# Performance work log

Measured on AMD Instinct MI355X. Metric: run time of the kernel, lower is better.

The kernel has to match this reference:

```python
import jax, jax.numpy as jnp
import numpy as np

WINDOW_SIZE = 11
SIGMA = 1.5
CHANNELS = 3
DATA_RANGE = 1.0


def _create_window(window_size, channel):
    x = np.arange(window_size) - window_size // 2
    g = np.exp(-(x ** 2) / (2.0 * SIGMA ** 2))
    g = g / g.sum()
    w2d = np.outer(g, g).astype(np.float32)  # [ws, ws]
    # depthwise kernel, OIHW with I=1, O=channel
    return jnp.asarray(np.broadcast_to(w2d, (channel, 1, window_size, window_size)).copy())


def _depthwise_conv(x, window, channel):
    # x: [B, C, H, W], window: [C, 1, ws, ws], VALID padding, groups=C
    return jax.lax.conv_general_dilated(
        x, window, window_strides=(1, 1), padding='VALID',
        dimension_numbers=('NCHW', 'OIHW', 'NCHW'),
        feature_group_count=channel)


def setup_inputs() -> dict:
    key = jax.random.key(0)
    k1, k2 = jax.random.split(key)
    img1 = jax.random.uniform(k1, (32, CHANNELS, 512, 512), dtype=jnp.float32)
    img2 = jax.random.uniform(k2, (32, CHANNELS, 512, 512), dtype=jnp.float32)
    return {"img1": img1, "img2": img2}


def reference(img1, img2):
    channel = img1.shape[1]
    window = _create_window(WINDOW_SIZE, channel).astype(img1.dtype)

    mu1 = _depthwise_conv(img1, window, channel)
    mu2 = _depthwise_conv(img2, window, channel)
    mu1_sq = mu1 * mu1
    mu2_sq = mu2 * mu2
    mu1_mu2 = mu1 * mu2

    sigma1_sq = _depthwise_conv(img1 * img1, window, channel) - mu1_sq
    sigma2_sq = _depthwise_conv(img2 * img2, window, channel) - mu2_sq
    sigma12 = _depthwise_conv(img1 * img2, window, channel) - mu1_mu2

    C1 = (0.01 * DATA_RANGE) ** 2
    C2 = (0.03 * DATA_RANGE) ** 2
    v1 = 2.0 * sigma12 + C2
    v2 = sigma1_sq + sigma2_sq + C2
    ssim_map = (2.0 * mu1_mu2 + C1) * v1 / ((mu1_sq + mu2_sq + C1) * v2)
    # mean over channel, height, width -> per-image SSIM [B]
    return ssim_map.mean(axis=(1, 2, 3))
```

## Files before the change

kernel.cpp:

```cpp
#include <hip/hip_runtime.h>
#include <math.h>

#define H 512
#define W 512
#define OUT_H 502
#define OUT_W 502
#define C1c 1.0e-4f
#define C2c 9.0e-4f

#define TH 111
#define NR 121
#define HALO 10
#define SPAN 64
#define SLOTW 76

__global__ __launch_bounds__(256, 4)
void ssim_kernel(const float* __restrict__ img1,
                 const float* __restrict__ img2,
                 float* __restrict__ out) {
    __shared__ float4 stg[4][SLOTW];
    __shared__ float wsum[4];

    const int tid  = threadIdx.x;
    const int wid  = tid >> 6;
    const int lane = tid & 63;

    float g[11];
    {
        float s = 0.f;
#pragma unroll
        for (int i = 0; i < 11; ++i) {
            float d = (float)(i - 5);
            g[i] = expf(-d * d * (1.0f / 4.5f));
            s += g[i];
        }
        float inv = 1.0f / s;
#pragma unroll
        for (int i = 0; i < 11; ++i) {
            g[i] *= inv;
            g[i] = __uint_as_float(__builtin_amdgcn_readfirstlane(__float_as_uint(g[i])));
        }
    }

    const int base = blockIdx.x * 256 + wid * SPAN;
    const int oyb  = blockIdx.y * TH;
    const int Y0   = min(oyb, H - NR);
    const int plane = blockIdx.z;
    const size_t pbase = (size_t)plane * (H * W);
    const float* __restrict__ p1 = img1 + pbase;
    const float* __restrict__ p2 = img2 + pbase;

    const int gx = base + lane;
    const int hx = min(base + SPAN + lane, W - 1);
    const float cmask = (gx < OUT_W) ? 1.0f : 0.0f;
    const bool hl = (lane < HALO);

    float4* const st = stg[wid];

    float a0[11], a1[11], a2[11], a3[11], a4[11];
#pragma unroll
    for (int i = 0; i < 11; ++i) { a0[i]=0.f; a1[i]=0.f; a2[i]=0.f; a3[i]=0.f; a4[i]=0.f; }

    float lsum = 0.f;

    int ro = Y0 * W;
    const int rocap = (H - 1) * W;

    float m1v = p1[ro + gx], m2v = p2[ro + gx];
    float h1v = 0.f, h2v = 0.f;
    if (hl) { h1v = p1[ro + hx]; h2v = p2[ro + hx]; }

#pragma unroll 1
    for (int rb = 0; rb < NR; rb += 11) {
#pragma unroll
        for (int p = 0; p < 11; ++p) {
            const int r = rb + p;

            st[lane] = make_float4(m1v, m2v, m1v * m2v, m1v * m1v);
            if (hl) st[SPAN + lane] = make_float4(h1v, h2v, h1v * h2v, h1v * h1v);

            ro = min(ro + W, rocap);
            m1v = p1[ro + gx]; m2v = p2[ro + gx];
            if (hl) { h1v = p1[ro + hx]; h2v = p2[ro + hx]; }

            __builtin_amdgcn_wave_barrier();

            float h0, h1, h2, h3, h4;
            {
                const float4* rp = st + lane;
#pragma unroll
                for (int t = 0; t < 11; ++t) {
                    const float4 v = rp[t];
                    const float w = g[t];
                    const float q22 = v.y * v.y;
                    if (t == 0) {
                        h0 = w * v.x; h1 = w * v.y; h2 = w * v.w;
                        h3 = w * q22; h4 = w * v.z;
                    } else {
                        h0 = fmaf(w, v.x, h0);
                        h1 = fmaf(w, v.y, h1);
                        h2 = fmaf(w, v.w, h2);
                        h3 = fmaf(w, q22, h3);
                        h4 = fmaf(w, v.z, h4);
                    }
                }
            }

            __builtin_amdgcn_wave_barrier();

#pragma unroll
            for (int a = 0; a < 11; ++a) {
                const float w = g[(p - a + 11) % 11];
                if (a == p) {
                    a0[a] = w * h0; a1[a] = w * h1; a2[a] = w * h2;
                    a3[a] = w * h3; a4[a] = w * h4;
                } else {
                    a0[a] = fmaf(w, h0, a0[a]); a1[a] = fmaf(w, h1, a1[a]);
                    a2[a] = fmaf(w, h2, a2[a]); a3[a] = fmaf(w, h3, a3[a]);
                    a4[a] = fmaf(w, h4, a4[a]);
                }
            }

            if (r >= 10) {
                const int e = (p + 1) % 11;
                const int oy = Y0 + r - 10;
                if (oy >= oyb) {
                    const float m1 = a0[e], m2 = a1[e];
                    const float m1s = m1 * m1, m2s = m2 * m2, m12 = m1 * m2;
                    const float sig1  = a2[e] - m1s;
                    const float sig2  = a3[e] - m2s;
                    const float sig12 = a4[e] - m12;
                    const float num = (2.f * m12 + C1c) * (2.f * sig12 + C2c);
                    const float den = (m1s + m2s + C1c) * (sig1 + sig2 + C2c);
                    const float v = num * __builtin_amdgcn_rcpf(den);
                    lsum = fmaf(cmask, v, lsum);
                }
            }
        }
    }

#pragma unroll
    for (int off = 32; off > 0; off >>= 1) lsum += __shfl_down(lsum, off, 64);
    if (lane == 0) wsum[wid] = lsum;
    __syncthreads();
    if (tid == 0) {
        const float inv_count = 1.0f / (3.0f * (float)OUT_H * (float)OUT_W);
        const float total = (wsum[0] + wsum[1] + wsum[2] + wsum[3]) * inv_count;
        atomicAdd(&out[plane / 3], total);
    }
}

__global__ void zero_out(float* out, int n) {
    int i = threadIdx.x + blockIdx.x * blockDim.x;
    if (i < n) out[i] = 0.f;
}

extern "C" void kernel_launch(void* const* d_in, const int* in_sizes, int n_in,
                              void* d_out, int out_size, void* d_ws, size_t ws_size,
                              hipStream_t stream) {
    const float* img1 = (const float*)d_in[0];
    const float* img2 = (const float*)d_in[1];
    float* out = (float*)d_out;

    zero_out<<<1, 64, 0, stream>>>(out, out_size);

    const int nplanes = in_sizes[0] / (H * W);
    dim3 grid(W / 256,
              (OUT_H + TH - 1) / TH,
              nplanes);
    ssim_kernel<<<grid, 256, 0, stream>>>(img1, img2, out);
}
```

Before: 275.5 us.

## Process two rows per iteration with double LDS staging and taller tiles

Each iteration of the sliding-window loop now stages and horizontally convolves two input rows into separate LDS buffers, and feeds both into the vertical ring accumulators. Tile height grows from 111 to 144 output rows, so halo re-reads shrink and there are fewer blocks. The aim is to halve the wave barriers and loop overhead per row and to expose more independent loads and FMAs. The cost is more registers and fewer blocks for occupancy and load balance, plus a rocap clamp change that could affect the last rows.

```diff
diff --git a/kernel.cpp b/kernel.cpp
--- a/kernel.cpp
+++ b/kernel.cpp
@@ -8,17 +8,17 @@
 #define C1c 1.0e-4f
 #define C2c 9.0e-4f
 
-#define TH 111
-#define NR 121
+#define TH 144
+#define NR 154
 #define HALO 10
 #define SPAN 64
-#define SLOTW 76
+#define SLOTQ 80
 
 __global__ __launch_bounds__(256, 4)
 void ssim_kernel(const float* __restrict__ img1,
                  const float* __restrict__ img2,
                  float* __restrict__ out) {
-    __shared__ float4 stg[4][SLOTW];
+    __shared__ float4 stg[4][2][SLOTQ];
     __shared__ float wsum[4];
 
     const int tid  = threadIdx.x;
@@ -55,53 +55,81 @@
     const float cmask = (gx < OUT_W) ? 1.0f : 0.0f;
     const bool hl = (lane < HALO);
 
-    float4* const st = stg[wid];
-
-    float a0[11], a1[11], a2[11], a3[11], a4[11];
-#pragma unroll
-    for (int i = 0; i < 11; ++i) { a0[i]=0.f; a1[i]=0.f; a2[i]=0.f; a3[i]=0.f; a4[i]=0.f; }
+    const float* __restrict__ q1  = p1 + gx;
+    const float* __restrict__ q2  = p2 + gx;
+    const float* __restrict__ qh1 = p1 + hx;
+    const float* __restrict__ qh2 = p2 + hx;
+
+    float4* const stA = stg[wid][0];
+    float4* const stB = stg[wid][1];
+
+    float a0[11], a1q[11], a2q[11], a3q[11], a4q[11];
+#pragma unroll
+    for (int i = 0; i < 11; ++i) { a0[i]=0.f; a1q[i]=0.f; a2q[i]=0.f; a3q[i]=0.f; a4q[i]=0.f; }
 
     float lsum = 0.f;
 
     int ro = Y0 * W;
-    const int rocap = (H - 1) * W;
-
-    float m1v = p1[ro + gx], m2v = p2[ro + gx];
-    float h1v = 0.f, h2v = 0.f;
-    if (hl) { h1v = p1[ro + hx]; h2v = p2[ro + hx]; }
+    const int rocap = (H - 2) * W;
+
+    float a1 = q1[ro],     a2 = q2[ro];
+    float b1 = q1[ro + W], b2 = q2[ro + W];
+    float ha1 = 0.f, ha2 = 0.f, hb1 = 0.f, hb2 = 0.f;
+    if (hl) { ha1 = qh1[ro]; ha2 = qh2[ro]; hb1 = qh1[ro + W]; hb2 = qh2[ro + W]; }
 
 #pragma unroll 1
-    for (int rb = 0; rb < NR; rb += 11) {
-#pragma unroll
-        for (int p = 0; p < 11; ++p) {
-            const int r = rb + p;
-
-            st[lane] = make_float4(m1v, m2v, m1v * m2v, m1v * m1v);
-            if (hl) st[SPAN + lane] = make_float4(h1v, h2v, h1v * h2v, h1v * h1v);
-
-            ro = min(ro + W, rocap);
-            m1v = p1[ro + gx]; m2v = p2[ro + gx];
-            if (hl) { h1v = p1[ro + hx]; h2v = p2[ro + hx]; }
+    for (int rb = 0; rb < NR; rb += 22) {
+#pragma unroll
+        for (int i = 0; i < 11; ++i) {
+            const int p  = (2 * i) % 11;
+            const int pp = (p + 1) % 11;
+            const int r  = rb + 2 * i;
+
+            stA[lane] = make_float4(a1, a2, a1 * a2, a1 * a1);
+            stB[lane] = make_float4(b1, b2, b1 * b2, b1 * b1);
+            if (hl) {
+                stA[SPAN + lane] = make_float4(ha1, ha2, ha1 * ha2, ha1 * ha1);
+                stB[SPAN + lane] = make_float4(hb1, hb2, hb1 * hb2, hb1 * hb1);
+            }
+
+            ro = min(ro + 2 * W, rocap);
+            a1 = q1[ro];     a2 = q2[ro];
+            b1 = q1[ro + W]; b2 = q2[ro + W];
+            if (hl) { ha1 = qh1[ro]; ha2 = qh2[ro]; hb1 = qh1[ro + W]; hb2 = qh2[ro + W]; }
 
             __builtin_amdgcn_wave_barrier();
 
-            float h0, h1, h2, h3, h4;
+            float hA0, hA1, hA2, hA3, hA4;
+            float hB0, hB1, hB2, hB3, hB4;
             {
-                const float4* rp = st + lane;
+                const float4* ra = stA + lane;
+                const float4* rb2 = stB + lane;
 #pragma unroll
                 for (int t = 0; t < 11; ++t) {
-                    const float4 v = rp[t];
+                    const float4 v = ra[t];
                     const float w = g[t];
                     const float q22 = v.y * v.y;
                     if (t == 0) {
-                        h0 = w * v.x; h1 = w * v.y; h2 = w * v.w;
-                        h3 = w * q22; h4 = w * v.z;
+                        hA0 = w * v.x; hA1 = w * v.y; hA2 = w * v.w;
+                        hA3 = w * q22; hA4 = w * v.z;
                     } else {
-                        h0 = fmaf(w, v.x, h0);
-                        h1 = fmaf(w, v.y, h1);
-                        h2 = fmaf(w, v.w, h2);
-                        h3 = fmaf(w, q22, h3);
-                        h4 = fmaf(w, v.z, h4);
+                        hA0 = fmaf(w, v.x, hA0); hA1 = fmaf(w, v.y, hA1);
+                        hA2 = fmaf(w, v.w, hA2); hA3 = fmaf(w, q22, hA3);
+                        hA4 = fmaf(w, v.z, hA4);
+                    }
+                }
+#pragma unroll
+                for (int t = 0; t < 11; ++t) {
+                    const float4 v = rb2[t];
+                    const float w = g[t];
+                    const float q22 = v.y * v.y;
+                    if (t == 0) {
+                        hB0 = w * v.x; hB1 = w * v.y; hB2 = w * v.w;
+                        hB3 = w * q22; hB4 = w * v.z;
+                    } else {
+                        hB0 = fmaf(w, v.x, hB0); hB1 = fmaf(w, v.y, hB1);
+                        hB2 = fmaf(w, v.w, hB2); hB3 = fmaf(w, q22, hB3);
+                        hB4 = fmaf(w, v.z, hB4);
                     }
                 }
             }
@@ -112,28 +140,54 @@
             for (int a = 0; a < 11; ++a) {
                 const float w = g[(p - a + 11) % 11];
                 if (a == p) {
-                    a0[a] = w * h0; a1[a] = w * h1; a2[a] = w * h2;
-                    a3[a] = w * h3; a4[a] = w * h4;
+                    a0[a] = w * hA0; a1q[a] = w * hA1; a2q[a] = w * hA2;
+                    a3q[a] = w * hA3; a4q[a] = w * hA4;
                 } else {
-                    a0[a] = fmaf(w, h0, a0[a]); a1[a] = fmaf(w, h1, a1[a]);
-                    a2[a] = fmaf(w, h2, a2[a]); a3[a] = fmaf(w, h3, a3[a]);
-                    a4[a] = fmaf(w, h4, a4[a]);
+                    a0[a]  = fmaf(w, hA0, a0[a]);  a1q[a] = fmaf(w, hA1, a1q[a]);
+                    a2q[a] = fmaf(w, hA2, a2q[a]); a3q[a] = fmaf(w, hA3, a3q[a]);
+                    a4q[a] = fmaf(w, hA4, a4q[a]);
                 }
             }
 
             if (r >= 10) {
-                const int e = (p + 1) % 11;
                 const int oy = Y0 + r - 10;
                 if (oy >= oyb) {
-                    const float m1 = a0[e], m2 = a1[e];
+                    const float m1 = a0[pp], m2 = a1q[pp];
                     const float m1s = m1 * m1, m2s = m2 * m2, m12 = m1 * m2;
-                    const float sig1  = a2[e] - m1s;
-                    const float sig2  = a3[e] - m2s;
-                    const float sig12 = a4[e] - m12;
+                    const float sig1  = a2q[pp] - m1s;
+                    const float sig2  = a3q[pp] - m2s;
+                    const float sig12 = a4q[pp] - m12;
                     const float num = (2.f * m12 + C1c) * (2.f * sig12 + C2c);
                     const float den = (m1s + m2s + C1c) * (sig1 + sig2 + C2c);
-                    const float v = num * __builtin_amdgcn_rcpf(den);
-                    lsum = fmaf(cmask, v, lsum);
+                    lsum = fmaf(cmask, num * __builtin_amdgcn_rcpf(den), lsum);
+                }
+            }
+
+#pragma unroll
+            for (int a = 0; a < 11; ++a) {
+                const float w = g[(pp - a + 11) % 11];
+                if (a == pp) {
+                    a0[a] = w * hB0; a1q[a] = w * hB1; a2q[a] = w * hB2;
+                    a3q[a] = w * hB3; a4q[a] = w * hB4;
+                } else {
+                    a0[a]  = fmaf(w, hB0, a0[a]);  a1q[a] = fmaf(w, hB1, a1q[a]);
+                    a2q[a] = fmaf(w, hB2, a2q[a]); a3q[a] = fmaf(w, hB3, a3q[a]);
+                    a4q[a] = fmaf(w, hB4, a4q[a]);
+                }
+            }
+
+            if (r >= 10) {
+                const int e2 = (p + 2) % 11;
+                const int oy2 = Y0 + r - 9;
+                if (oy2 >= oyb) {
+                    const float m1 = a0[e2], m2 = a1q[e2];
+                    const float m1s = m1 * m1, m2s = m2 * m2, m12 = m1 * m2;
+                    const float sig1  = a2q[e2] - m1s;
+                    const float sig2  = a3q[e2] - m2s;
+                    const float sig12 = a4q[e2] - m12;
+                    const float num = (2.f * m12 + C1c) * (2.f * sig12 + C2c);
+                    const float den = (m1s + m2s + C1c) * (sig1 + sig2 + C2c);
+                    lsum = fmaf(cmask, num * __builtin_amdgcn_rcpf(den), lsum);
                 }
             }
         }
```

Measured after the change: 482.1 us. 1.75x slower.
